# Kernel optimization log

Measured on AMD Instinct MI355X. Metric: run time of the kernel, lower is better.

Reference implementation:

```python
import jax, jax.numpy as jnp
import numpy as np

INPUT_SIZE = 512   # num_embeddings == RNN input feature dim
SEQ = INPUT_SIZE // 4   # 128, embedding dim == RNN seq_len
HID = 12
OUT = 3
B = 2048


def setup_inputs() -> dict:
    key = jax.random.key(0)
    ks = jax.random.split(key, 12)
    s = 0.1
    x = jax.random.randint(ks[0], (B, INPUT_SIZE), 0, INPUT_SIZE)
    emb = jax.random.normal(ks[1], (INPUT_SIZE, SEQ), dtype=jnp.float32) * s
    w_ih_f = jax.random.normal(ks[2], (HID, INPUT_SIZE), dtype=jnp.float32) * s
    w_hh_f = jax.random.normal(ks[3], (HID, HID), dtype=jnp.float32) * s
    b_ih_f = jax.random.normal(ks[4], (HID,), dtype=jnp.float32) * s
    b_hh_f = jax.random.normal(ks[5], (HID,), dtype=jnp.float32) * s
    w_ih_r = jax.random.normal(ks[6], (HID, INPUT_SIZE), dtype=jnp.float32) * s
    w_hh_r = jax.random.normal(ks[7], (HID, HID), dtype=jnp.float32) * s
    b_ih_r = jax.random.normal(ks[8], (HID,), dtype=jnp.float32) * s
    b_hh_r = jax.random.normal(ks[9], (HID,), dtype=jnp.float32) * s
    fc_w = jax.random.normal(ks[10], (OUT, 2 * HID), dtype=jnp.float32) * s
    fc_b = jax.random.normal(ks[11], (OUT,), dtype=jnp.float32) * s
    return {"x": x, "emb": emb,
            "w_ih_f": w_ih_f, "w_hh_f": w_hh_f, "b_ih_f": b_ih_f, "b_hh_f": b_hh_f,
            "w_ih_r": w_ih_r, "w_hh_r": w_hh_r, "b_ih_r": b_ih_r, "b_hh_r": b_hh_r,
            "fc_w": fc_w, "fc_b": fc_b}


def reference(x, emb, w_ih_f, w_hh_f, b_ih_f, b_hh_f,
              w_ih_r, w_hh_r, b_ih_r, b_hh_r, fc_w, fc_b):
    # embedding lookup: (B, INPUT_SIZE) -> (B, INPUT_SIZE, SEQ)
    e = emb[x]
    # view(-1, input_size, seq) is a no-op on this contiguous shape; swapaxes(1,2)
    xs = jnp.swapaxes(e, 1, 2)  # (B, SEQ, INPUT_SIZE): seq_len=SEQ, feat=INPUT_SIZE

    # forward-direction tanh RNN: precompute input projections, scan the recurrence
    pre = jnp.einsum('bsi,hi->sbh', xs, w_ih_f) + b_ih_f  # (SEQ, B, HID)

    def step(h, p):
        h = jnp.tanh(p + h @ w_hh_f.T + b_hh_f)
        return h, None

    h0 = jnp.zeros((xs.shape[0], HID), dtype=xs.dtype)
    h_fwd, _ = jax.lax.scan(step, h0, pre)  # final forward hidden (B, HID)

    # reverse-direction output at the LAST timestep = one step from zero hidden
    # on x_{T-1} (only out[:, -1, :] is consumed by the module)
    h_bwd = jnp.tanh(xs[:, -1, :] @ w_ih_r.T + b_ih_r + b_hh_r)  # (B, HID)

    out_last = jnp.concatenate([h_fwd, h_bwd], axis=-1)  # (B, 2*HID)
    return out_last @ fc_w.T + fc_b  # (B, OUT)
```

## Files before the change

### kernel.cpp

```cpp
#include <hip/hip_runtime.h>
#include <hip/hip_bf16.h>

#define B_N     2048
#define IN_N    512
#define SEQ_N   128
#define HID_N   12
#define HP_N    16
#define OUT_N   3

typedef __attribute__((ext_vector_type(8))) short short8;
typedef __attribute__((ext_vector_type(4))) float f32x4;
typedef __attribute__((ext_vector_type(4))) _Float16 f16x4;
typedef unsigned int uint;
typedef unsigned short ushort;

__device__ __forceinline__ float fast_tanh(float x) {
    float e = __builtin_amdgcn_exp2f(x * 2.8853900817779268f);
    return 1.0f - 2.0f * __builtin_amdgcn_rcpf(e + 1.0f);
}

__device__ __forceinline__ float tanh_ps(float x) {
    float e = __builtin_amdgcn_exp2f(x);
    return 1.0f - 2.0f * __builtin_amdgcn_rcpf(e + 1.0f);
}

__device__ __forceinline__ ushort f2bf(float f) {
    uint u = __float_as_uint(f);
    u += 0x7fffu + ((u >> 16) & 1u);
    return (ushort)(u >> 16);
}

__device__ __forceinline__ float bf2f(ushort s) {
    return __uint_as_float(((uint)s) << 16);
}

__global__ __launch_bounds__(256) void k_prep(
    const float* __restrict__ emb, const float* __restrict__ w_ih_f,
    const float* __restrict__ w_ih_r,
    ushort* __restrict__ embB, ushort* __restrict__ wP)
{
    int tid = blockIdx.x * 256 + threadIdx.x;
    float4 e = ((const float4*)emb)[tid];
    uint2 o;
    o.x = (uint)f2bf(e.x) | ((uint)f2bf(e.y) << 16);
    o.y = (uint)f2bf(e.z) | ((uint)f2bf(e.w) << 16);
    ((uint2*)embB)[tid] = o;

    int j   = tid & 7;
    int l   = (tid >> 3) & 63;
    int src = (tid >> 9) & 1;
    int cks = tid >> 10;
    int h   = l & 15;
    int i   = (cks >> 2) * 128 + (cks & 3) * 32 + (l >> 4) * 8 + j;
    const float* wsrc = src ? w_ih_r : w_ih_f;
    wP[(((size_t)cks * 2 + src) * 64 + l) * 8 + j] =
        (h < HID_N) ? f2bf(wsrc[h * IN_N + i]) : (ushort)0;
}

__global__ __launch_bounds__(256, 2) void k_pre(
    const int* __restrict__ x, const ushort* __restrict__ embB,
    const ushort* __restrict__ wP,
    const float* __restrict__ b_ih_r, const float* __restrict__ b_hh_r,
    ushort* __restrict__ preB, float* __restrict__ rev)
{
    __shared__ __align__(16) ushort As[128 * 128];
    __shared__ __align__(16) ushort wPs[16384];

    const int t      = threadIdx.x;
    const int l      = t & 63;
    const int w      = t >> 6;
    const int lane16 = l & 15;
    const int quad   = l >> 4;
    const int il     = w * 32 + quad * 8;
    const int wg     = w * 4 + quad;
    const int l7     = lane16 & 7;
    const int so     = lane16 * 8;
    const int b0     = blockIdx.x * 4;

    {
        const uint4* s4 = (const uint4*)wP;
        uint4*       d4 = (uint4*)wPs;
        #pragma unroll
        for (int i = 0; i < 8; ++i) d4[t + i * 256] = s4[t + i * 256];
    }

    f32x4 a0_0={0.f,0.f,0.f,0.f}, a0_1={0.f,0.f,0.f,0.f}, a0_2={0.f,0.f,0.f,0.f}, a0_3={0.f,0.f,0.f,0.f};
    f32x4 a1_0={0.f,0.f,0.f,0.f}, a1_1={0.f,0.f,0.f,0.f}, a1_2={0.f,0.f,0.f,0.f}, a1_3={0.f,0.f,0.f,0.f};
    f32x4 aR_0={0.f,0.f,0.f,0.f}, aR_1={0.f,0.f,0.f,0.f}, aR_2={0.f,0.f,0.f,0.f}, aR_3={0.f,0.f,0.f,0.f};

    uint RA[8][4], RB[8][4];
    int4 IA0, IA1, IB0, IB1;

#define IDXLD(Ilo, Ihi, bq2, c2) do { \
    const int* xq_ = x + (size_t)(b0 + (bq2)) * IN_N + (c2) * 128 + il; \
    Ilo = *(const int4*)xq_;  Ihi = *(const int4*)(xq_ + 4); \
} while (0)

#define GFETCH(Rb, Ilo, Ihi) do { uint4 v_; \
    v_ = *(const uint4*)(embB + (size_t)(Ilo).x * SEQ_N + so); Rb[0][0]=v_.x; Rb[0][1]=v_.y; Rb[0][2]=v_.z; Rb[0][3]=v_.w; \
    v_ = *(const uint4*)(embB + (size_t)(Ilo).y * SEQ_N + so); Rb[1][0]=v_.x; Rb[1][1]=v_.y; Rb[1][2]=v_.z; Rb[1][3]=v_.w; \
    v_ = *(const uint4*)(embB + (size_t)(Ilo).z * SEQ_N + so); Rb[2][0]=v_.x; Rb[2][1]=v_.y; Rb[2][2]=v_.z; Rb[2][3]=v_.w; \
    v_ = *(const uint4*)(embB + (size_t)(Ilo).w * SEQ_N + so); Rb[3][0]=v_.x; Rb[3][1]=v_.y; Rb[3][2]=v_.z; Rb[3][3]=v_.w; \
    v_ = *(const uint4*)(embB + (size_t)(Ihi).x * SEQ_N + so); Rb[4][0]=v_.x; Rb[4][1]=v_.y; Rb[4][2]=v_.z; Rb[4][3]=v_.w; \
    v_ = *(const uint4*)(embB + (size_t)(Ihi).y * SEQ_N + so); Rb[5][0]=v_.x; Rb[5][1]=v_.y; Rb[5][2]=v_.z; Rb[5][3]=v_.w; \
    v_ = *(const uint4*)(embB + (size_t)(Ihi).z * SEQ_N + so); Rb[6][0]=v_.x; Rb[6][1]=v_.y; Rb[6][2]=v_.z; Rb[6][3]=v_.w; \
    v_ = *(const uint4*)(embB + (size_t)(Ihi).w * SEQ_N + so); Rb[7][0]=v_.x; Rb[7][1]=v_.y; Rb[7][2]=v_.z; Rb[7][3]=v_.w; \
} while (0)

#define PACKR(Rb) do { \
    _Pragma("unroll") \
    for (int pp = 0; pp < 8; ++pp) { \
        const uint sel_ = (pp & 1) ? 0x07060302u : 0x05040100u; \
        const int pv_ = pp >> 1; \
        uint u0_ = __builtin_amdgcn_perm(Rb[1][pv_], Rb[0][pv_], sel_); \
        uint u1_ = __builtin_amdgcn_perm(Rb[3][pv_], Rb[2][pv_], sel_); \
        uint u2_ = __builtin_amdgcn_perm(Rb[5][pv_], Rb[4][pv_], sel_); \
        uint u3_ = __builtin_amdgcn_perm(Rb[7][pv_], Rb[6][pv_], sel_); \
        const int s_    = lane16 * 8 + pp; \
        const int slot_ = wg ^ pp ^ l7; \
        *(uint4*)&As[(size_t)s_ * 128 + (size_t)slot_ * 8] = make_uint4(u0_, u1_, u2_, u3_); \
    } \
} while (0)

#define MMA(A0, A1, AR) do { \
    _Pragma("unroll") \
    for (int tt = 0; tt < 2; ++tt) { \
        const int row_ = (w * 2 + tt) * 16 + lane16; \
        const int fr_  = (row_ & 7) ^ ((row_ >> 3) & 7); \
        _Pragma("unroll") \
        for (int ks = 0; ks < 4; ++ks) { \
            const int slot_ = (ks * 4 + quad) ^ fr_; \
            short8 af_ = *(const short8*)&As[(size_t)row_ * 128 + (size_t)slot_ * 8]; \
            if (tt == 0) { A0 = __builtin_amdgcn_mfma_f32_16x16x32_bf16(af_, bfr[ks], A0, 0, 0, 0); } \
            else { A1 = __builtin_amdgcn_mfma_f32_16x16x32_bf16(af_, bfr[ks], A1, 0, 0, 0); \
                   AR = __builtin_amdgcn_mfma_f32_16x16x32_bf16(af_, bfrR[ks], AR, 0, 0, 0); } \
        } \
    } \
} while (0)

    IDXLD(IA0, IA1, 0, 0);
    IDXLD(IB0, IB1, 1, 0);
    GFETCH(RA, IA0, IA1);
    GFETCH(RB, IB0, IB1);
    IDXLD(IA0, IA1, 2, 0);

    for (int c = 0; c < 4; ++c) {
        short8 bfr[4], bfrR[4];
        #pragma unroll
        for (int bq = 0; bq < 4; ++bq) {
            if (bq & 1) PACKR(RB); else PACKR(RA);

            if (!(c == 3 && bq >= 2)) {
                if (bq & 1) GFETCH(RB, IB0, IB1); else GFETCH(RA, IA0, IA1);
            }
            if (!(c == 3 && bq >= 1)) {
                if      (bq == 0) IDXLD(IB0, IB1, 3, c);
                else if (bq == 1) IDXLD(IA0, IA1, 0, c + 1);
                else if (bq == 2) IDXLD(IB0, IB1, 1, c + 1);
                else              IDXLD(IA0, IA1, 2, c + 1);
            }

            asm volatile("s_waitcnt lgkmcnt(0)" ::: "memory");
            __builtin_amdgcn_s_barrier();
            __builtin_amdgcn_sched_barrier(0);

            if (bq == 0) {
                #pragma unroll
                for (int ks = 0; ks < 4; ++ks) {
                    const ushort* wp = wPs + (size_t)((c * 4 + ks) * 128 + l) * 8;
                    bfr[ks]  = *(const short8*)wp;
                    bfrR[ks] = *(const short8*)(wp + 512);
                }
            }

            if      (bq == 0) MMA(a0_0, a1_0, aR_0);
            else if (bq == 1) MMA(a0_1, a1_1, aR_1);
            else if (bq == 2) MMA(a0_2, a1_2, aR_2);
            else              MMA(a0_3, a1_3, aR_3);

            asm volatile("" ::: "memory");
            __builtin_amdgcn_s_barrier();
            __builtin_amdgcn_sched_barrier(0);
        }
    }

#define EPI(bq, A0, A1, AR) do { \
    const int bcur_ = b0 + (bq); \
    _Pragma("unroll") \
    for (int r = 0; r < 4; ++r) { \
        const int s0_ = (w * 2 + 0) * 16 + quad * 4 + r; \
        preB[((size_t)bcur_ * SEQ_N + s0_) * HP_N + lane16] = f2bf(A0[r]); \
        const int s1_ = (w * 2 + 1) * 16 + quad * 4 + r; \
        preB[((size_t)bcur_ * SEQ_N + s1_) * HP_N + lane16] = f2bf(A1[r]); \
    } \
    if (w == 3 && quad == 3) \
        rev[bcur_ * HP_N + lane16] = fast_tanh(AR[3] + b_ih_r[lane16] + b_hh_r[lane16]); \
} while (0)

    if (lane16 < HID_N) {
        EPI(0, a0_0, a1_0, aR_0);
        EPI(1, a0_1, a1_1, aR_1);
        EPI(2, a0_2, a1_2, aR_2);
        EPI(3, a0_3, a1_3, aR_3);
    }
#undef IDXLD
#undef GFETCH
#undef PACKR
#undef MMA
#undef EPI
}

__global__ __launch_bounds__(256) void k_rnn(
    const ushort* __restrict__ preB, const float* __restrict__ rev,
    const float* __restrict__ w_hh_f,
    const float* __restrict__ b_ih_f, const float* __restrict__ b_hh_f,
    const float* __restrict__ fc_w, const float* __restrict__ fc_b,
    float* __restrict__ out)
{
    __shared__ float ho[64][16];

    const int t      = threadIdx.x;
    const int l      = t & 63;
    const int wv     = t >> 6;
    const int lane16 = l & 15;
    const int quad   = l >> 4;
    const int bloc   = wv * 16 + lane16;
    const int b      = blockIdx.x * 64 + bloc;

    const float SC = 2.8853900817779268f;

    f16x4 aW;
    {
        float w0_=0.f, w1_=0.f, w2_=0.f, w3_=0.f;
        if (lane16 < HID_N && quad < 3) {
            const float* wr = w_hh_f + lane16 * 12 + quad * 4;
            w0_ = wr[0]; w1_ = wr[1]; w2_ = wr[2]; w3_ = wr[3];
        }
        aW[0] = (_Float16)(SC * w0_);
        aW[1] = (_Float16)(SC * w1_);
        aW[2] = (_Float16)(SC * w2_);
        aW[3] = (_Float16)(SC * w3_);
    }

    float bias0=0.f, bias1=0.f, bias2=0.f, bias3=0.f;
    if (quad < 3) {
        const int h = quad * 4;
        bias0 = SC * (b_ih_f[h]     + b_hh_f[h]);
        bias1 = SC * (b_ih_f[h + 1] + b_hh_f[h + 1]);
        bias2 = SC * (b_ih_f[h + 2] + b_hh_f[h + 2]);
        bias3 = SC * (b_ih_f[h + 3] + b_hh_f[h + 3]);
    }

    const ushort* pb = preB + (size_t)b * SEQ_N * HP_N + quad * 4;
    uint2 pq[16];
    #pragma unroll
    for (int k = 0; k < 16; ++k) pq[k] = *(const uint2*)(pb + k * HP_N);

    f16x4 hB = {(_Float16)0.f, (_Float16)0.f, (_Float16)0.f, (_Float16)0.f};
    float t0 = 0.f, t1 = 0.f, t2 = 0.f, t3 = 0.f;

    for (int s16 = 0; s16 < 8; ++s16) {
        #pragma unroll
        for (int k = 0; k < 16; ++k) {
            const int s = s16 * 16 + k;
            uint2 pv = pq[k];
            float c0 = __builtin_fmaf(bf2f((ushort)(pv.x & 0xffffu)), SC, bias0);
            float c1 = __builtin_fmaf(bf2f((ushort)(pv.x >> 16)),     SC, bias1);
            float c2 = __builtin_fmaf(bf2f((ushort)(pv.y & 0xffffu)), SC, bias2);
            float c3 = __builtin_fmaf(bf2f((ushort)(pv.y >> 16)),     SC, bias3);
            if (quad == 3) { c0 = 0.f; c1 = 0.f; c2 = 0.f; c3 = 0.f; }
            pq[k] = *(const uint2*)(pb + ((s + 16) & 127) * HP_N);
            f32x4 cc = {c0, c1, c2, c3};
            f32x4 d = __builtin_amdgcn_mfma_f32_16x16x16f16(aW, hB, cc, 0, 0, 0);
            t0 = tanh_ps(d[0]);
            t1 = tanh_ps(d[1]);
            t2 = tanh_ps(d[2]);
            t3 = tanh_ps(d[3]);
            f16x4 nh;
            nh[0] = (_Float16)t0;
            nh[1] = (_Float16)t1;
            nh[2] = (_Float16)t2;
            nh[3] = (_Float16)t3;
            hB = nh;
        }
    }

    *(float4*)&ho[bloc][quad * 4] = make_float4(t0, t1, t2, t3);
    if (quad == 0) {
        float4 h0 = *(const float4*)&ho[bloc][0];
        float4 h1 = *(const float4*)&ho[bloc][4];
        float4 h2 = *(const float4*)&ho[bloc][8];
        float hv[12] = {h0.x,h0.y,h0.z,h0.w, h1.x,h1.y,h1.z,h1.w,
                        h2.x,h2.y,h2.z,h2.w};
        const float* rv = rev + b * HP_N;
        float rvv[12];
        #pragma unroll
        for (int k2 = 0; k2 < 12; ++k2) rvv[k2] = rv[k2];
        #pragma unroll
        for (int o = 0; o < OUT_N; ++o) {
            const float* fw = fc_w + o * 24;
            float acc = fc_b[o];
            #pragma unroll
            for (int k2 = 0; k2 < 12; ++k2)
                acc += fw[k2] * hv[k2] + fw[12 + k2] * rvv[k2];
            out[b * OUT_N + o] = acc;
        }
    }
}

extern "C" void kernel_launch(void* const* d_in, const int* in_sizes, int n_in,
                              void* d_out, int out_size, void* d_ws, size_t ws_size,
                              hipStream_t stream) {
    const int*   x      = (const int*)  d_in[0];
    const float* emb    = (const float*)d_in[1];
    const float* w_ih_f = (const float*)d_in[2];
    const float* w_hh_f = (const float*)d_in[3];
    const float* b_ih_f = (const float*)d_in[4];
    const float* b_hh_f = (const float*)d_in[5];
    const float* w_ih_r = (const float*)d_in[6];
    const float* b_ih_r = (const float*)d_in[8];
    const float* b_hh_r = (const float*)d_in[9];
    const float* fc_w   = (const float*)d_in[10];
    const float* fc_b   = (const float*)d_in[11];
    float* out = (float*)d_out;

    ushort* preB = (ushort*)d_ws;
    float*  rev  = (float*)((char*)d_ws + 8388608);
    ushort* embB = (ushort*)((char*)d_ws + 8519680);
    ushort* wP   = (ushort*)((char*)d_ws + 8650752);

    k_prep<<<64,    256, 0, stream>>>(emb, w_ih_f, w_ih_r, embB, wP);
    k_pre <<<B_N/4, 256, 0, stream>>>(x, embB, wP, b_ih_r, b_hh_r, preB, rev);
    k_rnn <<<B_N/64,256, 0, stream>>>(preB, rev, w_hh_f, b_ih_f, b_hh_f, fc_w, fc_b, out);
}
```

Before: 116.2 us.

## Transpose gathered embeddings in registers via identity MFMA, one batch row per wave

Rewrites the input-projection kernel so each wave handles one batch row. The gathered embedding rows are transposed in registers by multiplying with identity matrices through MFMA, then fed into 16x16x16 f16 MFMAs against the input weights. This replaces the shared-memory transpose staging buffer and its per-step barriers, and switches the embedding and weight copies from bf16 to fp16. The cost is extra MFMA work for the identity transposes, an f32 to f16 round trip, and fp16 range and precision instead of bf16.

```diff
diff --git a/kernel.cpp b/kernel.cpp
--- a/kernel.cpp
+++ b/kernel.cpp
@@ -11,6 +11,7 @@
 typedef __attribute__((ext_vector_type(8))) short short8;
 typedef __attribute__((ext_vector_type(4))) float f32x4;
 typedef __attribute__((ext_vector_type(4))) _Float16 f16x4;
+typedef __attribute__((ext_vector_type(8))) _Float16 f16x8;
 typedef unsigned int uint;
 typedef unsigned short ushort;
 
@@ -41,20 +42,18 @@
 {
     int tid = blockIdx.x * 256 + threadIdx.x;
     float4 e = ((const float4*)emb)[tid];
-    uint2 o;
-    o.x = (uint)f2bf(e.x) | ((uint)f2bf(e.y) << 16);
-    o.y = (uint)f2bf(e.z) | ((uint)f2bf(e.w) << 16);
-    ((uint2*)embB)[tid] = o;
-
-    int j   = tid & 7;
-    int l   = (tid >> 3) & 63;
-    int src = (tid >> 9) & 1;
-    int cks = tid >> 10;
-    int h   = l & 15;
-    int i   = (cks >> 2) * 128 + (cks & 3) * 32 + (l >> 4) * 8 + j;
-    const float* wsrc = src ? w_ih_r : w_ih_f;
-    wP[(((size_t)cks * 2 + src) * 64 + l) * 8 + j] =
-        (h < HID_N) ? f2bf(wsrc[h * IN_N + i]) : (ushort)0;
+    f16x4 hv = {(_Float16)e.x, (_Float16)e.y, (_Float16)e.z, (_Float16)e.w};
+    ((f16x4*)embB)[tid] = hv;
+
+    int j     = tid & 3;
+    int l     = (tid >> 2) & 63;
+    int src   = (tid >> 8) & 1;
+    int istep = tid >> 9;
+    int h     = l & 15;
+    int i     = istep * 16 + (l >> 4) * 4 + j;
+    const float* ws = src ? w_ih_r : w_ih_f;
+    _Float16 v = (h < HID_N) ? (_Float16)ws[h * IN_N + i] : (_Float16)0.f;
+    ((_Float16*)wP)[((size_t)(istep * 2 + src) * 64 + l) * 4 + j] = v;
 }
 
 __global__ __launch_bounds__(256, 2) void k_pre(
@@ -63,151 +62,99 @@
     const float* __restrict__ b_ih_r, const float* __restrict__ b_hh_r,
     ushort* __restrict__ preB, float* __restrict__ rev)
 {
-    __shared__ __align__(16) ushort As[128 * 128];
     __shared__ __align__(16) ushort wPs[16384];
+    __shared__ int xbs[4][IN_N];
 
     const int t      = threadIdx.x;
     const int l      = t & 63;
-    const int w      = t >> 6;
+    const int wv     = t >> 6;
     const int lane16 = l & 15;
     const int quad   = l >> 4;
-    const int il     = w * 32 + quad * 8;
-    const int wg     = w * 4 + quad;
-    const int l7     = lane16 & 7;
-    const int so     = lane16 * 8;
-    const int b0     = blockIdx.x * 4;
+    const int b      = blockIdx.x * 4 + wv;
 
     {
         const uint4* s4 = (const uint4*)wP;
         uint4*       d4 = (uint4*)wPs;
         #pragma unroll
         for (int i = 0; i < 8; ++i) d4[t + i * 256] = s4[t + i * 256];
-    }
-
-    f32x4 a0_0={0.f,0.f,0.f,0.f}, a0_1={0.f,0.f,0.f,0.f}, a0_2={0.f,0.f,0.f,0.f}, a0_3={0.f,0.f,0.f,0.f};
-    f32x4 a1_0={0.f,0.f,0.f,0.f}, a1_1={0.f,0.f,0.f,0.f}, a1_2={0.f,0.f,0.f,0.f}, a1_3={0.f,0.f,0.f,0.f};
-    f32x4 aR_0={0.f,0.f,0.f,0.f}, aR_1={0.f,0.f,0.f,0.f}, aR_2={0.f,0.f,0.f,0.f}, aR_3={0.f,0.f,0.f,0.f};
-
-    uint RA[8][4], RB[8][4];
-    int4 IA0, IA1, IB0, IB1;
-
-#define IDXLD(Ilo, Ihi, bq2, c2) do { \
-    const int* xq_ = x + (size_t)(b0 + (bq2)) * IN_N + (c2) * 128 + il; \
-    Ilo = *(const int4*)xq_;  Ihi = *(const int4*)(xq_ + 4); \
-} while (0)
-
-#define GFETCH(Rb, Ilo, Ihi) do { uint4 v_; \
-    v_ = *(const uint4*)(embB + (size_t)(Ilo).x * SEQ_N + so); Rb[0][0]=v_.x; Rb[0][1]=v_.y; Rb[0][2]=v_.z; Rb[0][3]=v_.w; \
-    v_ = *(const uint4*)(embB + (size_t)(Ilo).y * SEQ_N + so); Rb[1][0]=v_.x; Rb[1][1]=v_.y; Rb[1][2]=v_.z; Rb[1][3]=v_.w; \
-    v_ = *(const uint4*)(embB + (size_t)(Ilo).z * SEQ_N + so); Rb[2][0]=v_.x; Rb[2][1]=v_.y; Rb[2][2]=v_.z; Rb[2][3]=v_.w; \
-    v_ = *(const uint4*)(embB + (size_t)(Ilo).w * SEQ_N + so); Rb[3][0]=v_.x; Rb[3][1]=v_.y; Rb[3][2]=v_.z; Rb[3][3]=v_.w; \
-    v_ = *(const uint4*)(embB + (size_t)(Ihi).x * SEQ_N + so); Rb[4][0]=v_.x; Rb[4][1]=v_.y; Rb[4][2]=v_.z; Rb[4][3]=v_.w; \
-    v_ = *(const uint4*)(embB + (size_t)(Ihi).y * SEQ_N + so); Rb[5][0]=v_.x; Rb[5][1]=v_.y; Rb[5][2]=v_.z; Rb[5][3]=v_.w; \
-    v_ = *(const uint4*)(embB + (size_t)(Ihi).z * SEQ_N + so); Rb[6][0]=v_.x; Rb[6][1]=v_.y; Rb[6][2]=v_.z; Rb[6][3]=v_.w; \
-    v_ = *(const uint4*)(embB + (size_t)(Ihi).w * SEQ_N + so); Rb[7][0]=v_.x; Rb[7][1]=v_.y; Rb[7][2]=v_.z; Rb[7][3]=v_.w; \
-} while (0)
-
-#define PACKR(Rb) do { \
-    _Pragma("unroll") \
-    for (int pp = 0; pp < 8; ++pp) { \
-        const uint sel_ = (pp & 1) ? 0x07060302u : 0x05040100u; \
-        const int pv_ = pp >> 1; \
-        uint u0_ = __builtin_amdgcn_perm(Rb[1][pv_], Rb[0][pv_], sel_); \
-        uint u1_ = __builtin_amdgcn_perm(Rb[3][pv_], Rb[2][pv_], sel_); \
-        uint u2_ = __builtin_amdgcn_perm(Rb[5][pv_], Rb[4][pv_], sel_); \
-        uint u3_ = __builtin_amdgcn_perm(Rb[7][pv_], Rb[6][pv_], sel_); \
-        const int s_    = lane16 * 8 + pp; \
-        const int slot_ = wg ^ pp ^ l7; \
-        *(uint4*)&As[(size_t)s_ * 128 + (size_t)slot_ * 8] = make_uint4(u0_, u1_, u2_, u3_); \
-    } \
-} while (0)
-
-#define MMA(A0, A1, AR) do { \
-    _Pragma("unroll") \
-    for (int tt = 0; tt < 2; ++tt) { \
-        const int row_ = (w * 2 + tt) * 16 + lane16; \
-        const int fr_  = (row_ & 7) ^ ((row_ >> 3) & 7); \
-        _Pragma("unroll") \
-        for (int ks = 0; ks < 4; ++ks) { \
-            const int slot_ = (ks * 4 + quad) ^ fr_; \
-            short8 af_ = *(const short8*)&As[(size_t)row_ * 128 + (size_t)slot_ * 8]; \
-            if (tt == 0) { A0 = __builtin_amdgcn_mfma_f32_16x16x32_bf16(af_, bfr[ks], A0, 0, 0, 0); } \
-            else { A1 = __builtin_amdgcn_mfma_f32_16x16x32_bf16(af_, bfr[ks], A1, 0, 0, 0); \
-                   AR = __builtin_amdgcn_mfma_f32_16x16x32_bf16(af_, bfrR[ks], AR, 0, 0, 0); } \
-        } \
-    } \
-} while (0)
-
-    IDXLD(IA0, IA1, 0, 0);
-    IDXLD(IB0, IB1, 1, 0);
-    GFETCH(RA, IA0, IA1);
-    GFETCH(RB, IB0, IB1);
-    IDXLD(IA0, IA1, 2, 0);
-
-    for (int c = 0; c < 4; ++c) {
-        short8 bfr[4], bfrR[4];
-        #pragma unroll
-        for (int bq = 0; bq < 4; ++bq) {
-            if (bq & 1) PACKR(RB); else PACKR(RA);
-
-            if (!(c == 3 && bq >= 2)) {
-                if (bq & 1) GFETCH(RB, IB0, IB1); else GFETCH(RA, IA0, IA1);
-            }
-            if (!(c == 3 && bq >= 1)) {
-                if      (bq == 0) IDXLD(IB0, IB1, 3, c);
-                else if (bq == 1) IDXLD(IA0, IA1, 0, c + 1);
-                else if (bq == 2) IDXLD(IB0, IB1, 1, c + 1);
-                else              IDXLD(IA0, IA1, 2, c + 1);
-            }
-
-            asm volatile("s_waitcnt lgkmcnt(0)" ::: "memory");
-            __builtin_amdgcn_s_barrier();
-            __builtin_amdgcn_sched_barrier(0);
-
-            if (bq == 0) {
-                #pragma unroll
-                for (int ks = 0; ks < 4; ++ks) {
-                    const ushort* wp = wPs + (size_t)((c * 4 + ks) * 128 + l) * 8;
-                    bfr[ks]  = *(const short8*)wp;
-                    bfrR[ks] = *(const short8*)(wp + 512);
-                }
-            }
-
-            if      (bq == 0) MMA(a0_0, a1_0, aR_0);
-            else if (bq == 1) MMA(a0_1, a1_1, aR_1);
-            else if (bq == 2) MMA(a0_2, a1_2, aR_2);
-            else              MMA(a0_3, a1_3, aR_3);
-
-            asm volatile("" ::: "memory");
-            __builtin_amdgcn_s_barrier();
-            __builtin_amdgcn_sched_barrier(0);
-        }
-    }
-
-#define EPI(bq, A0, A1, AR) do { \
-    const int bcur_ = b0 + (bq); \
-    _Pragma("unroll") \
-    for (int r = 0; r < 4; ++r) { \
-        const int s0_ = (w * 2 + 0) * 16 + quad * 4 + r; \
-        preB[((size_t)bcur_ * SEQ_N + s0_) * HP_N + lane16] = f2bf(A0[r]); \
-        const int s1_ = (w * 2 + 1) * 16 + quad * 4 + r; \
-        preB[((size_t)bcur_ * SEQ_N + s1_) * HP_N + lane16] = f2bf(A1[r]); \
-    } \
-    if (w == 3 && quad == 3) \
-        rev[bcur_ * HP_N + lane16] = fast_tanh(AR[3] + b_ih_r[lane16] + b_hh_r[lane16]); \
-} while (0)
+        const int4* xs = (const int4*)(x + (size_t)b * IN_N);
+        ((int4*)xbs[wv])[l]      = xs[l];
+        ((int4*)xbs[wv])[l + 64] = xs[l + 64];
+    }
+    __syncthreads();
+
+    f16x8 I1, I2;
+    #pragma unroll
+    for (int j = 0; j < 8; ++j) {
+        int k = quad * 8 + j;
+        I1[j] = (k == lane16)      ? (_Float16)1.f : (_Float16)0.f;
+        I2[j] = (k == lane16 + 16) ? (_Float16)1.f : (_Float16)0.f;
+    }
+
+    f32x4 acc[8];
+    #pragma unroll
+    for (int sc = 0; sc < 8; ++sc) acc[sc] = (f32x4){0.f, 0.f, 0.f, 0.f};
+    f32x4 accR = {0.f, 0.f, 0.f, 0.f};
+    const f32x4 zz = {0.f, 0.f, 0.f, 0.f};
+
+    uint4 G[3][4];
+
+    #pragma unroll
+    for (int ic = 0; ic < 3; ++ic) {
+        int row = xbs[wv][ic * 16 + lane16];
+        const ushort* rp = embB + (size_t)row * SEQ_N + quad * 8;
+        #pragma unroll
+        for (int w = 0; w < 4; ++w) G[ic][w] = *(const uint4*)(rp + w * 32);
+    }
+
+    f16x4 bwC = *(const f16x4*)&wPs[0 * 64 * 4 + l * 4];
+    f16x4 brC = *(const f16x4*)&wPs[1 * 64 * 4 + l * 4];
+
+    #pragma unroll
+    for (int ic = 0; ic < 32; ++ic) {
+        int nrow = 0;
+        if (ic + 3 < 32) nrow = xbs[wv][(ic + 3) * 16 + lane16];
+        f16x4 bwN = bwC, brN = brC;
+        if (ic + 1 < 32) {
+            bwN = *(const f16x4*)&wPs[(size_t)(((ic + 1) * 2 + 0) * 64 + l) * 4];
+            brN = *(const f16x4*)&wPs[(size_t)(((ic + 1) * 2 + 1) * 64 + l) * 4];
+        }
+
+        #pragma unroll
+        for (int w = 0; w < 4; ++w) {
+            f16x8 Af = *(f16x8*)&G[ic % 3][w];
+            f32x4 d1 = __builtin_amdgcn_mfma_f32_16x16x32_f16(Af, I1, zz, 0, 0, 0);
+            f32x4 d2 = __builtin_amdgcn_mfma_f32_16x16x32_f16(Af, I2, zz, 0, 0, 0);
+            f16x4 a1 = {(_Float16)d1[0], (_Float16)d1[1],
+                        (_Float16)d1[2], (_Float16)d1[3]};
+            f16x4 a2 = {(_Float16)d2[0], (_Float16)d2[1],
+                        (_Float16)d2[2], (_Float16)d2[3]};
+            acc[2 * w]     = __builtin_amdgcn_mfma_f32_16x16x16f16(a1, bwC, acc[2 * w],     0, 0, 0);
+            acc[2 * w + 1] = __builtin_amdgcn_mfma_f32_16x16x16f16(a2, bwC, acc[2 * w + 1], 0, 0, 0);
+            if (w == 3)
+                accR = __builtin_amdgcn_mfma_f32_16x16x16f16(a2, brC, accR, 0, 0, 0);
+        }
+
+        if (ic + 3 < 32) {
+            const ushort* rp = embB + (size_t)nrow * SEQ_N + quad * 8;
+            #pragma unroll
+            for (int w = 0; w < 4; ++w) G[ic % 3][w] = *(const uint4*)(rp + w * 32);
+        }
+        bwC = bwN; brC = brN;
+    }
 
     if (lane16 < HID_N) {
-        EPI(0, a0_0, a1_0, aR_0);
-        EPI(1, a0_1, a1_1, aR_1);
-        EPI(2, a0_2, a1_2, aR_2);
-        EPI(3, a0_3, a1_3, aR_3);
-    }
-#undef IDXLD
-#undef GFETCH
-#undef PACKR
-#undef MMA
-#undef EPI
+        #pragma unroll
+        for (int sc = 0; sc < 8; ++sc) {
+            #pragma unroll
+            for (int r = 0; r < 4; ++r)
+                preB[((size_t)b * SEQ_N + sc * 16 + quad * 4 + r) * HP_N + lane16] =
+                    f2bf(acc[sc][r]);
+        }
+        if (quad == 3)
+            rev[b * HP_N + lane16] =
+                fast_tanh(accR[3] + b_ih_r[lane16] + b_hh_r[lane16]);
+    }
 }
 
 __global__ __launch_bounds__(256) void k_rnn(
@@ -299,11 +246,11 @@
         #pragma unroll
         for (int o = 0; o < OUT_N; ++o) {
             const float* fw = fc_w + o * 24;
-            float acc = fc_b[o];
+            float accv = fc_b[o];
             #pragma unroll
             for (int k2 = 0; k2 < 12; ++k2)
-                acc += fw[k2] * hv[k2] + fw[12 + k2] * rvv[k2];
-            out[b * OUT_N + o] = acc;
+                accv += fw[k2] * hv[k2] + fw[12 + k2] * rvv[k2];
+            out[b * OUT_N + o] = accv;
         }
     }
 }
```

Result: slower. 132.4 us (+13.9%).
